# Performance work log

Hardware: AMD Instinct MI355X
Metric: run time of the kernel (lower is better)

The kernel has to match this reference:

```python
import jax, jax.numpy as jnp
import numpy as np

B, NQ, NC, C, NH, NP, DFF, HH, WW = 4, 300, 16, 256, 8, 4, 2048, 128, 128


def _ln(x, g, b):
    m = jnp.mean(x, -1, keepdims=True)
    v = jnp.mean((x - m) ** 2, -1, keepdims=True)
    return (x - m) / jnp.sqrt(v + 1e-5) * g + b


def _mha(x, wi, bi, wo, bo, n_heads):
    Bx, L, Cx = x.shape
    d = Cx // n_heads
    q, k, v = jnp.split(x @ wi.T + bi, 3, axis=-1)
    sh = lambda t: t.reshape(Bx, L, n_heads, d).transpose(0, 2, 1, 3)
    scale = float(1.0 / np.sqrt(d))
    a = jax.nn.softmax(jnp.einsum('bhqd,bhkd->bhqk', sh(q), sh(k)) * scale, axis=-1)
    o = jnp.einsum('bhqk,bhkd->bhqd', a, sh(v)).transpose(0, 2, 1, 3).reshape(Bx, L, Cx)
    return o @ wo.T + bo


def _grid_sample(im, grid):
    # im: [N, Ch, H, W]; grid: [N, L, P, 2] in [-1,1]; bilinear, zeros padding, align_corners=False
    N, Ch, H, W = im.shape
    gx = (grid[..., 0] + 1.0) * (W * 0.5) - 0.5
    gy = (grid[..., 1] + 1.0) * (H * 0.5) - 0.5
    x0 = jnp.floor(gx)
    y0 = jnp.floor(gy)
    wx1 = gx - x0
    wy1 = gy - y0
    imf = im.reshape(N, Ch, H * W)

    def gather(xi, yi):
        valid = ((xi >= 0) & (xi < W) & (yi >= 0) & (yi < H)).astype(im.dtype)
        idx = jnp.clip(yi, 0, H - 1).astype(jnp.int32) * W + jnp.clip(xi, 0, W - 1).astype(jnp.int32)
        vals = jnp.take_along_axis(imf, idx.reshape(N, 1, -1), axis=2).reshape(N, Ch, *xi.shape[1:])
        return vals * valid[:, None]

    return (gather(x0, y0) * ((1 - wx1) * (1 - wy1))[:, None]
            + gather(x0 + 1, y0) * (wx1 * (1 - wy1))[:, None]
            + gather(x0, y0 + 1) * ((1 - wx1) * wy1)[:, None]
            + gather(x0 + 1, y0 + 1) * (wx1 * wy1)[:, None])


def setup_inputs() -> dict:
    key = jax.random.key(0)
    ks = jax.random.split(key, 30)
    s = 0.02
    p = lambda k, shp: jax.random.normal(k, shp, jnp.float32) * s
    cxcy = jax.random.uniform(ks[0], (B, NQ * NC, 2), jnp.float32)
    wh = jax.random.uniform(ks[1], (B, NQ * NC, 2), jnp.float32) * 0.2 + 0.02
    return {
        'inst_query': jax.random.normal(ks[2], (B, NQ, C), jnp.float32),
        'sub_contour_query': jax.random.normal(ks[3], (B, NQ, NC, C), jnp.float32),
        'memory_feats': jax.random.normal(ks[4], (B, HH * WW, C), jnp.float32),
        'reference_boxes': jnp.concatenate([cxcy, wh], axis=-1),
        'inst_in_w': p(ks[5], (3 * C, C)), 'inst_in_b': p(ks[6], (3 * C,)),
        'inst_out_w': p(ks[7], (C, C)), 'inst_out_b': p(ks[8], (C,)),
        'sc_in_w': p(ks[9], (3 * C, C)), 'sc_in_b': p(ks[10], (3 * C,)),
        'sc_out_w': p(ks[11], (C, C)), 'sc_out_b': p(ks[12], (C,)),
        'off_w': p(ks[13], (NH * NP * 2, C)), 'off_b': p(ks[14], (NH * NP * 2,)),
        'aw_w': p(ks[15], (NH * NP, C)), 'aw_b': p(ks[16], (NH * NP,)),
        'outp_w': p(ks[17], (C, C)), 'outp_b': p(ks[18], (C,)),
        'lin1_w': p(ks[19], (DFF, C)), 'lin1_b': p(ks[20], (DFF,)),
        'lin2_w': p(ks[21], (C, DFF)), 'lin2_b': p(ks[22], (C,)),
        'n1_g': jnp.ones((C,), jnp.float32), 'n1_b': jnp.zeros((C,), jnp.float32),
        'n2_g': jnp.ones((C,), jnp.float32), 'n2_b': jnp.zeros((C,), jnp.float32),
        'n3_g': jnp.ones((C,), jnp.float32), 'n3_b': jnp.zeros((C,), jnp.float32),
        'H': HH, 'W': WW,
    }


def reference(inst_query, sub_contour_query, memory_feats, reference_boxes,
              inst_in_w, inst_in_b, inst_out_w, inst_out_b,
              sc_in_w, sc_in_b, sc_out_w, sc_out_b,
              off_w, off_b, aw_w, aw_b, outp_w, outp_b,
              lin1_w, lin1_b, lin2_w, lin2_b,
              n1_g, n1_b, n2_g, n2_b, n3_g, n3_b, H, W):
    Bx, Nq, Nc, Cx = sub_contour_query.shape
    Lq = Nq * Nc
    hd = Cx // NH
    # --- decoupled self-attention (eval mode: dropout = identity) ---
    inst_o = _mha(inst_query, inst_in_w, inst_in_b, inst_out_w, inst_out_b, NH)
    sc = sub_contour_query.transpose(0, 2, 1, 3).reshape(Bx * Nc, Nq, Cx)
    sc_o = _mha(sc, sc_in_w, sc_in_b, sc_out_w, sc_out_b, NH)
    sc_o = sc_o.reshape(Bx, Nc, Nq, Cx).transpose(0, 2, 1, 3)
    q_sa = sc_o + inst_o[:, :, None, :]
    tgt = (sub_contour_query + q_sa).reshape(Bx, Lq, Cx)
    tgt = _ln(tgt + q_sa.reshape(Bx, Lq, Cx), n1_g, n1_b)
    # --- deformable cross-attention ---
    offsets = (tgt @ off_w.T + off_b).reshape(Bx, Lq, NH, NP, 2)
    aw = jax.nn.softmax((tgt @ aw_w.T + aw_b).reshape(Bx, Lq, NH, NP), axis=-1)
    ref = reference_boxes[:, :, None, None, :]
    loc = ref[..., :2] + offsets * ref[..., 2:] * 0.5
    grid = (loc * 2.0 - 1.0).transpose(0, 2, 1, 3, 4).reshape(Bx * NH, Lq, NP, 2)
    mem = memory_feats.reshape(Bx, H, W, Cx).transpose(0, 3, 1, 2).reshape(Bx * NH, hd, H, W)
    samp = _grid_sample(mem, grid).reshape(Bx, NH, hd, Lq, NP).transpose(0, 3, 1, 4, 2)  # [B,Lq,nH,nP,hd]
    tgt2 = (samp * aw[..., None]).sum(3).reshape(Bx, Lq, Cx) @ outp_w.T + outp_b
    tgt = _ln(tgt + tgt2, n2_g, n2_b)
    # --- FFN ---
    tgt2 = jax.nn.relu(tgt @ lin1_w.T + lin1_b) @ lin2_w.T + lin2_b
    tgt = _ln(tgt + tgt2, n3_g, n3_b)
    return tgt.reshape(Bx, Nq, Nc, Cx)
```

## Files before the change

kernel.cpp:

```cpp
#include <hip/hip_runtime.h>
#include <hip/hip_bf16.h>
#include <math.h>


typedef unsigned short u16;
typedef unsigned int u32;
typedef __attribute__((ext_vector_type(4))) float f32x4;
typedef __attribute__((ext_vector_type(8))) short s16x8;

__device__ __forceinline__ float b2f(u16 u) {
    union { u32 u; float f; } v; v.u = ((u32)u) << 16; return v.f;
}
__device__ __forceinline__ u16 f2b(float f) {
    union { float f; u32 u; } v; v.f = f;
    u32 r = v.u + 0x7fffu + ((v.u >> 16) & 1u);
    return (u16)(r >> 16);
}
__device__ __forceinline__ u32 pkbf(float a, float b) {
    u32 r;
    asm("v_cvt_pk_bf16_f32 %0, %1, %2" : "=v"(r) : "v"(a), "v"(b));
    return r;
}

#define GLOAD_LDS16(g, l) \
    __builtin_amdgcn_global_load_lds((const __attribute__((address_space(1))) void*)(g), \
                                     (__attribute__((address_space(3))) void*)(l), 16, 0, 0)

struct CvtSeg { const float* src; u16* dst; int nv; };
struct Cvt8 { CvtSeg s[8]; };

__global__ __launch_bounds__(256) void cvt_multi(Cvt8 a, int totalv) {
    int v = blockIdx.x * 256 + threadIdx.x;
    if (v >= totalv) return;
    int si = 0;
    while (si < 7 && v >= a.s[si].nv) { v -= a.s[si].nv; ++si; }
    const float* src = a.s[si].src + (size_t)v * 8;
    u16* dst = a.s[si].dst + (size_t)v * 8;
    float4 x = *(const float4*)src;
    float4 y = *(const float4*)(src + 4);
    u16 u[8] = { f2b(x.x), f2b(x.y), f2b(x.z), f2b(x.w),
                 f2b(y.x), f2b(y.y), f2b(y.z), f2b(y.w) };
    *(uint4*)dst = *(const uint4*)u;
}

__global__ __launch_bounds__(256) void pack_offaw(
    const float* __restrict__ off_w, const float* __restrict__ off_b,
    const float* __restrict__ aw_w, const float* __restrict__ aw_b,
    u16* __restrict__ wout, float* __restrict__ bout)
{
    int r = blockIdx.x, c = threadIdx.x;
    float v = 0.f;
    if (r < 64) v = off_w[r * 256 + c];
    else if (r < 96) v = aw_w[(r - 64) * 256 + c];
    wout[r * 256 + c] = f2b(v);
    if (c == 0) bout[r] = (r < 64) ? off_b[r] : (r < 96 ? aw_b[r - 64] : 0.f);
}

template<int RELU, int OUTBF16, int TM>
__global__ __launch_bounds__(256) void gemm_mfma(
    const u16* __restrict__ A, const u16* __restrict__ W,
    const float* __restrict__ bias, void* __restrict__ Cout,
    int M, int N, int K)
{
    constexpr int MI = TM / 32;
    constexpr int AU = TM / 64;
    __shared__ u16 smem[TM * 32 + 128 * 32];
    u16* Asm = smem;
    u16* Bsm = smem + TM * 32;
    const int tid = threadIdx.x;
    const int wave = tid >> 6, lane = tid & 63;
    const int gx = gridDim.x;
    const int nwg = gx * gridDim.y;
    const int lid = blockIdx.y * gx + blockIdx.x;
    const int q8 = nwg >> 3, r8 = nwg & 7;
    const int xcd = lid & 7, sub = lid >> 3;
    const int logical = (xcd < r8 ? xcd * (q8 + 1) : r8 * (q8 + 1) + (xcd - r8) * q8) + sub;
    const int bm = (logical / gx) * TM, bn = (logical % gx) * 128;
    const int wr = (wave >> 1) * (TM / 2), wc = (wave & 1) * 64;
    const int fr = lane & 15;
    const int fk = (lane >> 4) * 8;
    f32x4 acc[MI][4] = {};

    for (int k0 = 0; k0 < K; k0 += 32) {
        __syncthreads();
#pragma unroll
        for (int c = 0; c < AU; ++c) {
            int b = (c * 256 + tid) * 16;
            int row = b >> 6;
            int ke = (b & 63) >> 1;
            int ra = bm + row; if (ra >= M) ra = M - 1;
            GLOAD_LDS16(A + (size_t)ra * K + k0 + ke, Asm + (c * 256 + wave * 64) * 8);
        }
#pragma unroll
        for (int c = 0; c < 2; ++c) {
            int b = (c * 256 + tid) * 16;
            int row = b >> 6;
            int ke = (b & 63) >> 1;
            int rb = bn + row;
            GLOAD_LDS16(W + (size_t)rb * K + k0 + ke, Bsm + (c * 256 + wave * 64) * 8);
        }
        __syncthreads();
        s16x8 af[MI], bf[4];
#pragma unroll
        for (int i = 0; i < MI; ++i)
            af[i] = *(const s16x8*)(Asm + (wr + i * 16 + fr) * 32 + fk);
#pragma unroll
        for (int i = 0; i < 4; ++i)
            bf[i] = *(const s16x8*)(Bsm + (wc + i * 16 + fr) * 32 + fk);
#pragma unroll
        for (int mi = 0; mi < MI; ++mi)
#pragma unroll
            for (int ni = 0; ni < 4; ++ni)
                acc[mi][ni] = __builtin_amdgcn_mfma_f32_16x16x32_bf16(
                    af[mi], bf[ni], acc[mi][ni], 0, 0, 0);
    }
    const int cc = lane & 15, cr4 = (lane >> 4) * 4;
    if (OUTBF16) {
#pragma unroll
        for (int p = 0; p < TM / 32; ++p) {
            const int base = p * 32;
            __syncthreads();
#pragma unroll
            for (int mi = 0; mi < MI; ++mi) {
                int rowoff = wr + mi * 16;
                if (rowoff < base || rowoff >= base + 32) continue;
#pragma unroll
                for (int ni = 0; ni < 4; ++ni) {
                    int col = wc + ni * 16 + cc;
                    float bv = bias[bn + col];
#pragma unroll
                    for (int j = 0; j < 4; ++j) {
                        float v = acc[mi][ni][j] + bv;
                        if (RELU) v = fmaxf(v, 0.f);
                        smem[(rowoff - base + cr4 + j) * 136 + col] = f2b(v);
                    }
                }
            }
            __syncthreads();
            for (int t = tid; t < 512; t += 256) {
                int row = t >> 4, ck = t & 15;
                int grow = bm + base + row;
                if (grow < M)
                    *(uint4*)((u16*)Cout + (size_t)grow * N + bn + ck * 8) =
                        *(const uint4*)&smem[row * 136 + ck * 8];
            }
        }
    } else {
#pragma unroll
        for (int mi = 0; mi < MI; ++mi) {
#pragma unroll
            for (int ni = 0; ni < 4; ++ni) {
                int col = bn + wc + ni * 16 + cc;
                float bv = bias[col];
#pragma unroll
                for (int j = 0; j < 4; ++j) {
                    int row = bm + wr + mi * 16 + cr4 + j;
                    if (row >= M) continue;
                    float v = acc[mi][ni][j] + bv;
                    if (RELU) v = fmaxf(v, 0.f);
                    ((float*)Cout)[(size_t)row * N + col] = v;
                }
            }
        }
    }
}

#define VIDX(d, k) ((((k) >> 3) ^ ((d) & 7)) * 8 + ((k) & 7))

__global__ __launch_bounds__(256) void attn_mfma(
    const u16* __restrict__ qkv, u16* __restrict__ O, int S)
{
    const int bh = blockIdx.x / S, seg = blockIdx.x % S;
    const int bi = bh >> 3, h = bh & 7;
    __shared__ u16 Ks[320][40];
    __shared__ u16 Vt[32][384];
    const int tid = threadIdx.x;

    for (int idx = tid; idx < 1200; idx += 256) {
        int k = idx >> 2, sub = idx & 3;
        const u16* kp = qkv + ((size_t)(bi * 300 + k)) * 768 + 256 + h * 32 + sub * 8;
        *(uint4*)&Ks[k][sub * 8] = *(const uint4*)kp;
    }
    for (int idx = tid; idx < 600; idx += 256) {
        int kp2 = idx >> 2, sub = idx & 3;
        int k0 = kp2 * 2;
        const u16* vp = qkv + ((size_t)(bi * 300 + k0)) * 768 + 512 + h * 32 + sub * 8;
        uint4 v0 = *(const uint4*)vp;
        uint4 v1 = *(const uint4*)(vp + 768);
        u16 a0[8], a1[8];
        *(uint4*)a0 = v0; *(uint4*)a1 = v1;
#pragma unroll
        for (int j = 0; j < 8; ++j) {
            int d = sub * 8 + j;
            *(u32*)&Vt[d][VIDX(d, k0)] = (u32)a0[j] | ((u32)a1[j] << 16);
        }
    }
    for (int idx = tid; idx < 320; idx += 256) {
        int d = idx & 31, k0 = 300 + (idx >> 5) * 2;
        *(u32*)&Vt[d][VIDX(d, k0)] = 0;
    }
    __syncthreads();

    const int lane = tid & 63, wave = tid >> 6;
    const int c = lane & 15, g = lane >> 4;
    const int fk = g * 8;
    const f32x4 zero = { 0.f, 0.f, 0.f, 0.f };
    const float SCL2 = 0.25505416f;
    const int sA = c + ((g & 1) << 5);
    const int sB = sA + 16;
    const bool hi = g >= 2;

    for (int qt = seg * 4 + wave; qt < 19; qt += 4 * S) {
        int qrow = qt * 16 + c; if (qrow > 299) qrow = 299;
        s16x8 afq = *(const s16x8*)(qkv + ((size_t)(bi * 300 + qrow)) * 768 + h * 32 + fk);
        f32x4 acc0 = zero, acc1 = zero;
        float m = -1e30f, l = 0.f;

        for (int kc = 0; kc < 10; ++kc) {
            const int kb = kc * 32;
            s16x8 ak0 = *(const s16x8*)&Ks[kb + c][fk];
            s16x8 ak1 = *(const s16x8*)&Ks[kb + 16 + c][fk];
            __builtin_amdgcn_s_setprio(1);
            f32x4 s0 = __builtin_amdgcn_mfma_f32_16x16x32_bf16(ak0, afq, zero, 0, 0, 0);
            f32x4 s1 = __builtin_amdgcn_mfma_f32_16x16x32_bf16(ak1, afq, zero, 0, 0, 0);
            __builtin_amdgcn_s_setprio(0);
            if (kb == 288) {
#pragma unroll
                for (int j = 0; j < 4; ++j) {
                    if (g == 3) s0[j] = -1e30f;
                    s1[j] = -1e30f;
                }
            }
            float cm = fmaxf(fmaxf(fmaxf(s0[0], s0[1]), fmaxf(s0[2], s0[3])),
                             fmaxf(fmaxf(s1[0], s1[1]), fmaxf(s1[2], s1[3])));
            cm = fmaxf(cm, __shfl_xor(cm, 16));
            cm = fmaxf(cm, __shfl_xor(cm, 32));
            float mn = fmaxf(m, cm);
            float corr = exp2f((m - mn) * SCL2);
            m = mn;
            float p0[4], p1[4];
#pragma unroll
            for (int j = 0; j < 4; ++j) {
                p0[j] = exp2f((s0[j] - m) * SCL2);
                p1[j] = exp2f((s1[j] - m) * SCL2);
            }
            float cs = (p0[0] + p0[1]) + (p0[2] + p0[3])
                     + (p1[0] + p1[1]) + (p1[2] + p1[3]);
            cs += __shfl_xor(cs, 16);
            cs += __shfl_xor(cs, 32);
            l = l * corr + cs;
            u32 w0 = pkbf(p0[0], p0[1]), w1 = pkbf(p0[2], p0[3]);
            u32 w2 = pkbf(p1[0], p1[1]), w3 = pkbf(p1[2], p1[3]);
            int x0 = __shfl((int)w0, sA), x1 = __shfl((int)w1, sA);
            int x2 = __shfl((int)w2, sA), x3 = __shfl((int)w3, sA);
            int y0 = __shfl((int)w0, sB), y1 = __shfl((int)w1, sB);
            int y2 = __shfl((int)w2, sB), y3 = __shfl((int)w3, sB);
            union { u32 w[4]; s16x8 v; } afp;
            afp.w[0] = hi ? (u32)x2 : (u32)x0;
            afp.w[1] = hi ? (u32)x3 : (u32)x1;
            afp.w[2] = hi ? (u32)y2 : (u32)y0;
            afp.w[3] = hi ? (u32)y3 : (u32)y1;
            float c0 = __shfl(corr, g * 4 + 0), c1 = __shfl(corr, g * 4 + 1);
            float c2 = __shfl(corr, g * 4 + 2), c3 = __shfl(corr, g * 4 + 3);
            acc0[0] *= c0; acc0[1] *= c1; acc0[2] *= c2; acc0[3] *= c3;
            acc1[0] *= c0; acc1[1] *= c1; acc1[2] *= c2; acc1[3] *= c3;
            s16x8 bv0 = *(const s16x8*)&Vt[c][VIDX(c, kb + fk)];
            s16x8 bv1 = *(const s16x8*)&Vt[16 + c][VIDX(16 + c, kb + fk)];
            __builtin_amdgcn_s_setprio(1);
            acc0 = __builtin_amdgcn_mfma_f32_16x16x32_bf16(afp.v, bv0, acc0, 0, 0, 0);
            acc1 = __builtin_amdgcn_mfma_f32_16x16x32_bf16(afp.v, bv1, acc1, 0, 0, 0);
            __builtin_amdgcn_s_setprio(0);
        }
        float l0 = __shfl(l, g * 4 + 0), l1 = __shfl(l, g * 4 + 1);
        float l2 = __shfl(l, g * 4 + 2), l3 = __shfl(l, g * 4 + 3);
        float lj[4] = { l0, l1, l2, l3 };
#pragma unroll
        for (int j = 0; j < 4; ++j) {
            int q = qt * 16 + g * 4 + j;
            if (q < 300) {
                float r = 1.f / lj[j];
                u16* op = O + ((size_t)(bi * 300 + q)) * 256 + h * 32;
                op[c]      = f2b(acc0[j] * r);
                op[16 + c] = f2b(acc1[j] * r);
            }
        }
    }
}

__global__ __launch_bounds__(256) void sc_transpose(
    const float* __restrict__ scq, u16* __restrict__ out)
{
    int row = blockIdx.x * 4 + (threadIdx.x >> 6);
    int c4 = (threadIdx.x & 63) * 4;
    int b = row / 4800;
    int rem = row % 4800;
    int nc = rem / 300, nq = rem % 300;
    float4 v = *(const float4*)(scq + ((size_t)((b * 300 + nq) * 16 + nc)) * 256 + c4);
    u16 u[4] = { f2b(v.x), f2b(v.y), f2b(v.z), f2b(v.w) };
    *(uint2*)(out + (size_t)row * 256 + c4) = *(const uint2*)u;
}

__global__ __launch_bounds__(256) void ln1_combine(
    const float* __restrict__ scq, const float* __restrict__ sco,
    const float* __restrict__ insto, const float* __restrict__ g,
    const float* __restrict__ bta, float* __restrict__ tgt,
    u16* __restrict__ tgtb)
{
    int row = blockIdx.x * 4 + (threadIdx.x >> 6);
    int c4 = (threadIdx.x & 63) * 4;
    int b = row / 4800;
    int rem = row % 4800;
    int nq = rem >> 4, nc = rem & 15;
    float4 a = *(const float4*)(scq + (size_t)row * 256 + c4);
    float4 s = *(const float4*)(sco + ((size_t)((b * 16 + nc) * 300 + nq)) * 256 + c4);
    float4 i = *(const float4*)(insto + ((size_t)(b * 300 + nq)) * 256 + c4);
    float4 v = { a.x + 2.f * (s.x + i.x), a.y + 2.f * (s.y + i.y),
                 a.z + 2.f * (s.z + i.z), a.w + 2.f * (s.w + i.w) };
    float sm = v.x + v.y + v.z + v.w;
    float s2 = v.x * v.x + v.y * v.y + v.z * v.z + v.w * v.w;
#pragma unroll
    for (int o = 32; o; o >>= 1) { sm += __shfl_xor(sm, o); s2 += __shfl_xor(s2, o); }
    float mean = sm * (1.f / 256.f);
    float rstd = 1.f / sqrtf(s2 * (1.f / 256.f) - mean * mean + 1e-5f);
    float4 gv = *(const float4*)(g + c4);
    float4 bv = *(const float4*)(bta + c4);
    float4 r = { (v.x - mean) * rstd * gv.x + bv.x, (v.y - mean) * rstd * gv.y + bv.y,
                 (v.z - mean) * rstd * gv.z + bv.z, (v.w - mean) * rstd * gv.w + bv.w };
    *(float4*)(tgt + (size_t)row * 256 + c4) = r;
    u16 u[4] = { f2b(r.x), f2b(r.y), f2b(r.z), f2b(r.w) };
    *(uint2*)(tgtb + (size_t)row * 256 + c4) = *(const uint2*)u;
}

__global__ __launch_bounds__(256) void ln_add(
    const float* __restrict__ x, const float* __restrict__ y,
    const float* __restrict__ g, const float* __restrict__ bta,
    float* __restrict__ dst, u16* __restrict__ bdst)
{
    int row = blockIdx.x * 4 + (threadIdx.x >> 6);
    int c4 = (threadIdx.x & 63) * 4;
    float4 a = *(const float4*)(x + (size_t)row * 256 + c4);
    float4 b = *(const float4*)(y + (size_t)row * 256 + c4);
    float4 v = { a.x + b.x, a.y + b.y, a.z + b.z, a.w + b.w };
    float sm = v.x + v.y + v.z + v.w;
    float s2 = v.x * v.x + v.y * v.y + v.z * v.z + v.w * v.w;
#pragma unroll
    for (int o = 32; o; o >>= 1) { sm += __shfl_xor(sm, o); s2 += __shfl_xor(s2, o); }
    float mean = sm * (1.f / 256.f);
    float rstd = 1.f / sqrtf(s2 * (1.f / 256.f) - mean * mean + 1e-5f);
    float4 gv = *(const float4*)(g + c4);
    float4 bv = *(const float4*)(bta + c4);
    float4 r = { (v.x - mean) * rstd * gv.x + bv.x, (v.y - mean) * rstd * gv.y + bv.y,
                 (v.z - mean) * rstd * gv.z + bv.z, (v.w - mean) * rstd * gv.w + bv.w };
    *(float4*)(dst + (size_t)row * 256 + c4) = r;
    if (bdst) {
        u16 u[4] = { f2b(r.x), f2b(r.y), f2b(r.z), f2b(r.w) };
        *(uint2*)(bdst + (size_t)row * 256 + c4) = *(const uint2*)u;
    }
}

__global__ __launch_bounds__(256) void deform_sample(
    const float* __restrict__ oaw, const float* __restrict__ refb,
    const float* __restrict__ mem, u16* __restrict__ samp)
{
    const int row = blockIdx.x;
    const int b = row / 4800;
    const int tid = threadIdx.x;
    const int h = tid >> 5;
    const float4 rb = *(const float4*)(refb + (size_t)row * 4);
    const float* base = oaw + (size_t)row * 128;
    float a0 = base[64 + h * 4 + 0], a1 = base[64 + h * 4 + 1];
    float a2 = base[64 + h * 4 + 2], a3 = base[64 + h * 4 + 3];
    float am = fmaxf(fmaxf(a0, a1), fmaxf(a2, a3));
    float e0 = __expf(a0 - am), e1 = __expf(a1 - am), e2 = __expf(a2 - am), e3 = __expf(a3 - am);
    float rs = 1.f / (e0 + e1 + e2 + e3);
    float wp[4] = { e0 * rs, e1 * rs, e2 * rs, e3 * rs };
    const float* op = base + h * 8;
    const float* mb = mem + (size_t)b * 16384 * 256 + tid;

    int offs[16];
    float wts[16];
#pragma unroll
    for (int p = 0; p < 4; ++p) {
        float gx = (rb.x + op[p * 2 + 0] * rb.z * 0.5f) * 128.f - 0.5f;
        float gy = (rb.y + op[p * 2 + 1] * rb.w * 0.5f) * 128.f - 0.5f;
        float x0f = floorf(gx), y0f = floorf(gy);
        int x0 = (int)x0f, y0 = (int)y0f;
        float wx1 = gx - x0f, wy1 = gy - y0f;
        float wx0 = 1.f - wx1, wy0 = 1.f - wy1;
        float vx0 = ((unsigned)x0 < 128u) ? 1.f : 0.f;
        float vx1 = ((unsigned)(x0 + 1) < 128u) ? 1.f : 0.f;
        float vy0 = ((unsigned)y0 < 128u) ? 1.f : 0.f;
        float vy1 = ((unsigned)(y0 + 1) < 128u) ? 1.f : 0.f;
        int xc0 = min(max(x0, 0), 127), xc1 = min(max(x0 + 1, 0), 127);
        int yc0 = min(max(y0, 0), 127), yc1 = min(max(y0 + 1, 0), 127);
        offs[p * 4 + 0] = (yc0 * 128 + xc0) << 8;
        offs[p * 4 + 1] = (yc0 * 128 + xc1) << 8;
        offs[p * 4 + 2] = (yc1 * 128 + xc0) << 8;
        offs[p * 4 + 3] = (yc1 * 128 + xc1) << 8;
        wts[p * 4 + 0] = wp[p] * wx0 * wy0 * vx0 * vy0;
        wts[p * 4 + 1] = wp[p] * wx1 * wy0 * vx1 * vy0;
        wts[p * 4 + 2] = wp[p] * wx0 * wy1 * vx0 * vy1;
        wts[p * 4 + 3] = wp[p] * wx1 * wy1 * vx1 * vy1;
    }
    float vals[16];
#pragma unroll
    for (int i = 0; i < 16; ++i) vals[i] = mb[offs[i]];
    float acc = 0.f;
#pragma unroll
    for (int i = 0; i < 16; ++i) acc = fmaf(vals[i], wts[i], acc);
    samp[(size_t)row * 256 + tid] = f2b(acc);
}

extern "C" void kernel_launch(void* const* d_in, const int* in_sizes, int n_in,
                              void* d_out, int out_size, void* d_ws, size_t ws_size,
                              hipStream_t stream) {
    const float* inst_query = (const float*)d_in[0];
    const float* sub_contour = (const float*)d_in[1];
    const float* memory_feats = (const float*)d_in[2];
    const float* ref_boxes = (const float*)d_in[3];
    const float* inst_in_w = (const float*)d_in[4];
    const float* inst_in_b = (const float*)d_in[5];
    const float* inst_out_w = (const float*)d_in[6];
    const float* inst_out_b = (const float*)d_in[7];
    const float* sc_in_w = (const float*)d_in[8];
    const float* sc_in_b = (const float*)d_in[9];
    const float* sc_out_w = (const float*)d_in[10];
    const float* sc_out_b = (const float*)d_in[11];
    const float* off_w = (const float*)d_in[12];
    const float* off_b = (const float*)d_in[13];
    const float* aw_w = (const float*)d_in[14];
    const float* aw_b = (const float*)d_in[15];
    const float* outp_w = (const float*)d_in[16];
    const float* outp_b = (const float*)d_in[17];
    const float* lin1_w = (const float*)d_in[18];
    const float* lin1_b = (const float*)d_in[19];
    const float* lin2_w = (const float*)d_in[20];
    const float* lin2_b = (const float*)d_in[21];
    const float* n1_g = (const float*)d_in[22];
    const float* n1_b = (const float*)d_in[23];
    const float* n2_g = (const float*)d_in[24];
    const float* n2_b = (const float*)d_in[25];
    const float* n3_g = (const float*)d_in[26];
    const float* n3_b = (const float*)d_in[27];

    u16* wsb = (u16*)d_ws;
    u16* qkv_b   = wsb;
    u16* xbuf_b  = qkv_b + 14745600;
    u16* obuf_b  = xbuf_b + 4915200;
    u16* tgt_b   = obuf_b + 4915200;
    u16* w_inst_in  = tgt_b + 4915200;
    u16* w_inst_out = w_inst_in + 196608;
    u16* w_sc_in    = w_inst_out + 65536;
    u16* w_sc_out   = w_sc_in + 196608;
    u16* w_outp     = w_sc_out + 65536;
    u16* w_lin1     = w_outp + 65536;
    u16* w_lin2     = w_lin1 + 524288;
    u16* w_offaw    = w_lin2 + 524288;
    u16* ffn1_b = qkv_b;
    u16* instq_b = tgt_b;
    float* fp    = (float*)(w_offaw + 32768);
    float* insto = fp;
    float* tgt   = insto + 307200;
    float* t2    = tgt + 4915200;
    float* oawb  = t2 + 4915200;
    float* b_offaw = oawb + 2457600;
    size_t base_bytes = (size_t)((char*)(b_offaw + 128) - (char*)d_ws);
    size_t ffn_off = (base_bytes + 255) & ~(size_t)255;
    u16* ffn1_full = (u16*)((char*)d_ws + ffn_off);
    bool full_ffn = ws_size >= ffn_off + (size_t)2 * 19200 * 2048;

    dim3 blk(256);

    Cvt8 ca;
    ca.s[0] = { inst_in_w,  w_inst_in,  196608 / 8 };
    ca.s[1] = { inst_out_w, w_inst_out, 65536 / 8 };
    ca.s[2] = { sc_in_w,    w_sc_in,    196608 / 8 };
    ca.s[3] = { sc_out_w,   w_sc_out,   65536 / 8 };
    ca.s[4] = { outp_w,     w_outp,     65536 / 8 };
    ca.s[5] = { lin1_w,     w_lin1,     524288 / 8 };
    ca.s[6] = { lin2_w,     w_lin2,     524288 / 8 };
    ca.s[7] = { inst_query, instq_b,    307200 / 8 };
    int totalv = (196608 * 2 + 65536 * 3 + 524288 * 2 + 307200) / 8;
    cvt_multi<<<(totalv + 255) / 256, blk, 0, stream>>>(ca, totalv);
    pack_offaw<<<128, blk, 0, stream>>>(off_w, off_b, aw_w, aw_b, w_offaw, b_offaw);

    gemm_mfma<0,1,128><<<dim3(6, 10), blk, 0, stream>>>(instq_b, w_inst_in, inst_in_b, qkv_b, 1200, 768, 256);
    attn_mfma<<<128, blk, 0, stream>>>(qkv_b, obuf_b, 4);
    gemm_mfma<0,0,64><<<dim3(2, 19), blk, 0, stream>>>(obuf_b, w_inst_out, inst_out_b, insto, 1200, 256, 256);
    sc_transpose<<<4800, blk, 0, stream>>>(sub_contour, xbuf_b);
    gemm_mfma<0,1,128><<<dim3(6, 150), blk, 0, stream>>>(xbuf_b, w_sc_in, sc_in_b, qkv_b, 19200, 768, 256);
    attn_mfma<<<1024, blk, 0, stream>>>(qkv_b, obuf_b, 2);
    gemm_mfma<0,0,64><<<dim3(2, 300), blk, 0, stream>>>(obuf_b, w_sc_out, sc_out_b, t2, 19200, 256, 256);
    ln1_combine<<<4800, blk, 0, stream>>>(sub_contour, t2, insto, n1_g, n1_b, tgt, tgt_b);
    gemm_mfma<0,0,64><<<dim3(1, 300), blk, 0, stream>>>(tgt_b, w_offaw, b_offaw, oawb, 19200, 128, 256);
    deform_sample<<<19200, blk, 0, stream>>>(oawb, ref_boxes, memory_feats, obuf_b);
    gemm_mfma<0,0,64><<<dim3(2, 300), blk, 0, stream>>>(obuf_b, w_outp, outp_b, t2, 19200, 256, 256);
    ln_add<<<4800, blk, 0, stream>>>(tgt, t2, n2_g, n2_b, tgt, tgt_b);
    if (full_ffn) {
        gemm_mfma<1,1,128><<<dim3(16, 150), blk, 0, stream>>>(tgt_b, w_lin1, lin1_b, ffn1_full, 19200, 2048, 256);
        gemm_mfma<0,0,64><<<dim3(2, 300), blk, 0, stream>>>(ffn1_full, w_lin2, lin2_b, t2, 19200, 256, 2048);
    } else {
        for (int c = 0; c < 2; ++c) {
            gemm_mfma<1,1,128><<<dim3(16, 75), blk, 0, stream>>>(tgt_b + (size_t)c * 9600 * 256, w_lin1, lin1_b, ffn1_b, 9600, 2048, 256);
            gemm_mfma<0,0,64><<<dim3(2, 150), blk, 0, stream>>>(ffn1_b, w_lin2, lin2_b, t2 + (size_t)c * 9600 * 256, 9600, 256, 2048);
        }
    }
    ln_add<<<4800, blk, 0, stream>>>(tgt, t2, n3_g, n3_b, (float*)d_out, nullptr);
}
```

Before: 331.8 us.

## Double GEMM K-tile to 64 with XOR-swizzled LDS layout

The MFMA GEMM now stages a 64-wide K slice per iteration instead of 32, which halves the number of barrier pairs and load rounds per K. The LDS layout uses an XOR swizzle of the 16-byte chunk index by row, applied on both the global-to-LDS copy and the fragment reads, so that row-strided fragment loads avoid bank conflicts. The change doubles shared memory per block, which may reduce occupancy.

Result: faster. 319.6 us (-3.7%).

```diff
diff --git a/kernel.cpp b/kernel.cpp
--- a/kernel.cpp
+++ b/kernel.cpp
@@ -63,10 +63,11 @@
     int M, int N, int K)
 {
     constexpr int MI = TM / 32;
-    constexpr int AU = TM / 64;
-    __shared__ u16 smem[TM * 32 + 128 * 32];
+    constexpr int CHA = TM * 64 / 2048;
+    constexpr int CHB = 4;
+    __shared__ u16 smem[(TM + 128) * 64];
     u16* Asm = smem;
-    u16* Bsm = smem + TM * 32;
+    u16* Bsm = smem + TM * 64;
     const int tid = threadIdx.x;
     const int wave = tid >> 6, lane = tid & 63;
     const int gx = gridDim.x;
@@ -78,41 +79,46 @@
     const int bm = (logical / gx) * TM, bn = (logical % gx) * 128;
     const int wr = (wave >> 1) * (TM / 2), wc = (wave & 1) * 64;
     const int fr = lane & 15;
-    const int fk = (lane >> 4) * 8;
+    const int g = lane >> 4;
+    const int sw = fr & 7;
     f32x4 acc[MI][4] = {};
 
-    for (int k0 = 0; k0 < K; k0 += 32) {
+    for (int k0 = 0; k0 < K; k0 += 64) {
         __syncthreads();
 #pragma unroll
-        for (int c = 0; c < AU; ++c) {
-            int b = (c * 256 + tid) * 16;
-            int row = b >> 6;
-            int ke = (b & 63) >> 1;
-            int ra = bm + row; if (ra >= M) ra = M - 1;
-            GLOAD_LDS16(A + (size_t)ra * K + k0 + ke, Asm + (c * 256 + wave * 64) * 8);
-        }
-#pragma unroll
-        for (int c = 0; c < 2; ++c) {
-            int b = (c * 256 + tid) * 16;
-            int row = b >> 6;
-            int ke = (b & 63) >> 1;
-            int rb = bn + row;
-            GLOAD_LDS16(W + (size_t)rb * K + k0 + ke, Bsm + (c * 256 + wave * 64) * 8);
+        for (int c = 0; c < CHA; ++c) {
+            int L = c * 256 + tid;
+            int r = L >> 3, p = L & 7;
+            int cc = p ^ (r & 7);
+            int ra = bm + r; if (ra >= M) ra = M - 1;
+            GLOAD_LDS16(A + (size_t)ra * K + k0 + cc * 8, Asm + (c * 256 + wave * 64) * 8);
+        }
+#pragma unroll
+        for (int c = 0; c < CHB; ++c) {
+            int L = c * 256 + tid;
+            int r = L >> 3, p = L & 7;
+            int cc = p ^ (r & 7);
+            int rb = bn + r;
+            GLOAD_LDS16(W + (size_t)rb * K + k0 + cc * 8, Bsm + (c * 256 + wave * 64) * 8);
         }
         __syncthreads();
-        s16x8 af[MI], bf[4];
-#pragma unroll
-        for (int i = 0; i < MI; ++i)
-            af[i] = *(const s16x8*)(Asm + (wr + i * 16 + fr) * 32 + fk);
-#pragma unroll
-        for (int i = 0; i < 4; ++i)
-            bf[i] = *(const s16x8*)(Bsm + (wc + i * 16 + fr) * 32 + fk);
-#pragma unroll
-        for (int mi = 0; mi < MI; ++mi)
-#pragma unroll
-            for (int ni = 0; ni < 4; ++ni)
-                acc[mi][ni] = __builtin_amdgcn_mfma_f32_16x16x32_bf16(
-                    af[mi], bf[ni], acc[mi][ni], 0, 0, 0);
+#pragma unroll
+        for (int kk = 0; kk < 2; ++kk) {
+            const int pc = (kk * 4 + g) ^ sw;
+            s16x8 af[MI], bf[4];
+#pragma unroll
+            for (int i = 0; i < MI; ++i)
+                af[i] = *(const s16x8*)(Asm + (wr + i * 16 + fr) * 64 + pc * 8);
+#pragma unroll
+            for (int i = 0; i < 4; ++i)
+                bf[i] = *(const s16x8*)(Bsm + (wc + i * 16 + fr) * 64 + pc * 8);
+#pragma unroll
+            for (int mi = 0; mi < MI; ++mi)
+#pragma unroll
+                for (int ni = 0; ni < 4; ++ni)
+                    acc[mi][ni] = __builtin_amdgcn_mfma_f32_16x16x32_bf16(
+                        af[mi], bf[ni], acc[mi][ni], 0, 0, 0);
+        }
     }
     const int cc = lane & 15, cr4 = (lane >> 4) * 4;
     if (OUTBF16) {
```
